# Kernel tuning notes

Hardware: AMD Instinct MI355X
Metric: run time of the kernel (lower is better)

The kernel has to match this reference:

```python
import jax, jax.numpy as jnp
import numpy as np

NS, NV = 48, 10
N_NODES, N_EDGES = 10000, 100000
N_EDGE_FEAT = 3 * NS  # 144
W_SS, W_VS, W_SV, W_VV = NS * NS, NV * NS, NS * NV, NV * NV
W_NUMEL = W_SS + W_VS + W_SV + W_VV  # 3364 = FullyConnectedTensorProduct.weight_numel
IN_DIM = NS + 3 * NV  # 78
EPS = 1e-5


def setup_inputs() -> dict:
    key = jax.random.key(0)
    ks = jax.random.split(key, 8)
    return {
        "node_attr": jax.random.normal(ks[0], (N_NODES, IN_DIM), jnp.float32),
        "edge_attr": jax.random.normal(ks[1], (N_EDGES, N_EDGE_FEAT), jnp.float32),
        "edge_sh": jax.random.normal(ks[2], (N_EDGES, 4), jnp.float32),
        "fc1_w": jax.random.normal(ks[3], (N_EDGE_FEAT, N_EDGE_FEAT), jnp.float32) / np.sqrt(N_EDGE_FEAT).astype(np.float32),
        "fc1_b": jnp.zeros((N_EDGE_FEAT,), jnp.float32),
        "fc2_w": jax.random.normal(ks[4], (N_EDGE_FEAT, W_NUMEL), jnp.float32) / np.sqrt(N_EDGE_FEAT).astype(np.float32),
        "fc2_b": jnp.zeros((W_NUMEL,), jnp.float32),
        "bn_weight": jnp.ones((NS + NV,), jnp.float32),
        "bn_bias": jnp.zeros((NS,), jnp.float32),
        "edge_index": jax.random.randint(ks[5], (2, N_EDGES), 0, N_NODES),
    }


def reference(node_attr, edge_attr, edge_sh, fc1_w, fc1_b, fc2_w, fc2_b, bn_weight, bn_bias, edge_index):
    edge_src, edge_dst = edge_index[0], edge_index[1]
    # --- gather node feats per edge, split into irreps ---
    x = node_attr[edge_dst]                      # [E, 78]
    xs = x[:, :NS]                               # [E, 48]  scalars (0e)
    xv = x[:, NS:].reshape(-1, NV, 3)            # [E, 10, 3] vectors (1o)
    s0 = edge_sh[:, 0]                           # [E]     sh 0e
    s1 = edge_sh[:, 1:4]                         # [E, 3]  sh 1o

    # --- per-edge TP weights from edge MLP ---
    w = jax.nn.relu(edge_attr @ fc1_w + fc1_b) @ fc2_w + fc2_b  # [E, 3364]
    w_ss = w[:, :W_SS].reshape(-1, NS, NS)
    w_vs = w[:, W_SS:W_SS + W_VS].reshape(-1, NV, NS)
    w_sv = w[:, W_SS + W_VS:W_SS + W_VS + W_SV].reshape(-1, NS, NV)
    w_vv = w[:, W_SS + W_VS + W_SV:].reshape(-1, NV, NV)

    # path normalization: 1/sqrt(mul_in * n_paths_into_output_irrep)
    a_ss = 1.0 / np.sqrt(NS * 2.0)
    a_vs = 1.0 / np.sqrt(NV * 2.0)
    a_sv = 1.0 / np.sqrt(NS * 2.0)
    a_vv = 1.0 / np.sqrt(NV * 2.0)

    # --- Clebsch-Gordan tensor product (fully connected, per-edge weights) ---
    # 0e (x) 0e -> 0e
    out_s = a_ss * jnp.einsum('ei,eio->eo', xs, w_ss) * s0[:, None]
    # 1o (x) 1o -> 0e  (CG = delta/sqrt(3))
    dot = jnp.einsum('eic,ec->ei', xv, s1) / np.sqrt(3.0)
    out_s = out_s + a_vs * jnp.einsum('ei,eio->eo', dot, w_vs)
    # 0e (x) 1o -> 1o
    out_v = a_sv * jnp.einsum('ei,eio->eo', xs, w_sv)[:, :, None] * s1[:, None, :]
    # 1o (x) 0e -> 1o
    out_v = out_v + a_vv * jnp.einsum('eic,eio->eoc', xv, w_vv) * s0[:, None, None]

    tp = jnp.concatenate([out_s, out_v.reshape(-1, 3 * NV)], axis=1)  # [E, 78]

    # --- scatter-mean to nodes ---
    sums = jax.ops.segment_sum(tp, edge_src, num_segments=N_NODES)
    cnt = jax.ops.segment_sum(jnp.ones((tp.shape[0],), tp.dtype), edge_src, num_segments=N_NODES)
    out = sums / jnp.maximum(cnt, 1.0)[:, None]

    # --- residual (in_dim == out_dim -> pad is a no-op) ---
    out = out + node_attr

    # --- equivariant batch norm (e3nn-style, batch statistics) ---
    os = out[:, :NS]
    ov = out[:, NS:].reshape(-1, NV, 3)
    mu = os.mean(0)
    var = os.var(0)
    os = (os - mu) / jnp.sqrt(var + EPS) * bn_weight[:NS] + bn_bias
    fn = (ov ** 2).sum(-1).mean(0) / 3.0  # component-normalized mean squared norm per channel
    ov = ov / jnp.sqrt(fn + EPS)[None, :, None] * bn_weight[NS:][None, :, None]
    return jnp.concatenate([os, ov.reshape(-1, 3 * NV)], axis=1)
```

## Files before the change

kernel.cpp:

```cpp
#include <hip/hip_runtime.h>
#include <hip/hip_bf16.h>

#define NS   48
#define NV   10
#define NEF  144
#define WN   3364
#define IND  78
#define NE   100000
#define NN   10000
#define EPS  1e-5f
#define HP   144
#define EB   128

#define A_SS 0.10206207261596575f
#define A_VS 0.22360679774997896f
#define A_SV 0.10206207261596575f
#define A_VV 0.22360679774997896f
#define RS3  0.5773502691896258f

typedef __attribute__((ext_vector_type(8)))  short  short8;
typedef __attribute__((ext_vector_type(16))) float  f32x16;
typedef __attribute__((ext_vector_type(4)))  int    int4v;
typedef __attribute__((ext_vector_type(4)))  float  float4v;
typedef __attribute__((ext_vector_type(2)))  float  float2v;

#define MFMA32(a,b,c) __builtin_amdgcn_mfma_f32_32x32x16_bf16((a),(b),(c),0,0,0)

#define TP_F    0
#define ST_F    7800000
#define CNT_F   7800160
#define OFFS_F  7810160
#define CUR_F   7820164
#define EL_F    7830164
#define WSBF_F  7930168

#define OFF_W1  0
#define OFF_B1  23040
#define OFF_B2  468480
#define OFF_B3  561664
#define N_PREP  608256

__device__ __forceinline__ short tobf(float v) {
    return __builtin_bit_cast(short, __float2bfloat16(v));
}
__device__ __forceinline__ float fromb(short s) {
    unsigned u = ((unsigned)(unsigned short)s) << 16;
    return __builtin_bit_cast(float, u);
}
__device__ __forceinline__ unsigned pkt2(float a, float b) {
    unsigned ua = __builtin_bit_cast(unsigned, a);
    unsigned ub = __builtin_bit_cast(unsigned, b);
    return (ua >> 16) | (ub & 0xFFFF0000u);
}
__device__ __forceinline__ float waveReduceSum(float v) {
    #pragma unroll
    for (int o = 32; o > 0; o >>= 1) v += __shfl_down(v, o, 64);
    return v;
}
__device__ __forceinline__ void gl_lds16(const short* g, short* l) {
    __builtin_amdgcn_global_load_lds(
        (const __attribute__((address_space(1))) unsigned int*)g,
        (__attribute__((address_space(3))) unsigned int*)l, 16, 0, 0);
}

__global__ void prep_weights(const float* __restrict__ fc1_w,
                             const float* __restrict__ fc2_w,
                             const float* __restrict__ b2,
                             short* __restrict__ wsbf)
{
    int idx = blockIdx.x * 256 + threadIdx.x;
    if (idx >= N_PREP) return;
    float v = 0.f;
    if (idx < OFF_B1) {
        int r = idx;
        int tile = r / 4608, rem = r % 4608;
        int ks = rem / 512, l = (rem % 512) / 8, j = rem % 8;
        int n = tile * 32 + (l & 31);
        int k = ks * 16 + ((l >> 5) << 3) + j;
        v = (n < 144) ? fc1_w[k * 144 + n] : 0.f;
    } else if (idx < OFF_B2) {
        int r = idx - OFF_B1;
        if (r < 442368) {
            int i = r / 9216, rem = r % 9216;
            int tile = rem / 4608; rem %= 4608;
            int ks = rem / 512, l = (rem % 512) / 8, j = rem % 8;
            int n = tile * 32 + (l & 31);
            int k = ks * 16 + ((l >> 5) << 3) + j;
            if (n < 48)      v = fc2_w[(size_t)k * WN + i * 48 + n];
            else if (n < 58) v = fc2_w[(size_t)k * WN + 2784 + i * 10 + (n - 48)];
        } else {
            int rb = r - 442368;
            int tile = rb / 1536, rem = rb % 1536;
            int ks = rem / 512, l = (rem % 512) / 8, j = rem % 8;
            int n = tile * 32 + (l & 31);
            int k = ks * 16 + ((l >> 5) << 3) + j;
            if (n < 48)      v = b2[k * 48 + n];
            else if (n < 58) v = b2[2784 + k * 10 + (n - 48)];
        }
    } else if (idx < OFF_B3) {
        int r = idx - OFF_B2;
        if (r < 92160) {
            int i = r / 9216, rem = r % 9216;
            int tile = rem / 4608; rem %= 4608;
            int ks = rem / 512, l = (rem % 512) / 8, j = rem % 8;
            int n = tile * 32 + (l & 31);
            int k = ks * 16 + ((l >> 5) << 3) + j;
            if (n < 48) v = fc2_w[(size_t)k * WN + 2304 + i * 48 + n];
        } else {
            int rb = r - 92160;
            int tile = rb / 512, rem = rb % 512;
            int l = rem / 8, j = rem % 8;
            int n = tile * 32 + (l & 31);
            int k = ((l >> 5) << 3) + j;
            if (k < 10 && n < 48) v = b2[2304 + k * 48 + n];
        }
    } else {
        int r = idx - OFF_B3;
        if (r < 46080) {
            int i = r / 4608, rem = r % 4608;
            int ks = rem / 512, l = (rem % 512) / 8, j = rem % 8;
            int n = l & 31;
            int k = ks * 16 + ((l >> 5) << 3) + j;
            if (n < 10) v = fc2_w[(size_t)k * WN + 3264 + i * 10 + n];
        } else {
            int rb = r - 46080;
            int l = rb / 8, j = rb % 8;
            int n = l & 31;
            int k = ((l >> 5) << 3) + j;
            if (k < 10 && n < 10) v = b2[3264 + k * 10 + n];
        }
    }
    wsbf[idx] = tobf(v);
}

__global__ void hist_kernel(const int* __restrict__ eidx, int* __restrict__ cntI)
{
    int e = blockIdx.x * 256 + threadIdx.x;
    if (e < NE) atomicAdd(&cntI[eidx[e]], 1);
}

__global__ __launch_bounds__(1024) void scan_kernel(const int* __restrict__ cntI,
                                                    int* __restrict__ offs,
                                                    int* __restrict__ cursor)
{
    __shared__ int part[1024];
    int t = threadIdx.x;
    int base = t * 10;
    int local[10];
    int s = 0;
    #pragma unroll
    for (int q = 0; q < 10; ++q) {
        int i = base + q;
        int v = (i < NN) ? cntI[i] : 0;
        local[q] = s; s += v;
    }
    part[t] = s;
    __syncthreads();
    for (int o = 1; o < 1024; o <<= 1) {
        int v = (t >= o) ? part[t - o] : 0;
        __syncthreads();
        part[t] += v;
        __syncthreads();
    }
    int prev = (t == 0) ? 0 : part[t - 1];
    #pragma unroll
    for (int q = 0; q < 10; ++q) {
        int i = base + q;
        if (i < NN) { int val = prev + local[q]; offs[i] = val; cursor[i] = val; }
    }
    if (t == 1023) offs[NN] = part[1023];
}

__global__ void scatter_kernel(const int* __restrict__ eidx,
                               int* __restrict__ cursor, int* __restrict__ elist)
{
    int e = blockIdx.x * 256 + threadIdx.x;
    if (e < NE) {
        int pos = atomicAdd(&cursor[eidx[e]], 1);
        elist[pos] = e;
    }
}

__global__ __launch_bounds__(256, 2) void fused_main(
    const float* __restrict__ node_attr, const float* __restrict__ edge_attr,
    const float* __restrict__ edge_sh,   const float* __restrict__ b1,
    const int*   __restrict__ eidx,      const short* __restrict__ wsbf,
    float* __restrict__ tp)
{
    __shared__ short ubuf[18432];
    __shared__ short xfT[96 * EB];
    __shared__ float pbuf[EB][10];
    __shared__ float s0s[EB];
    __shared__ float s1s[EB][3];

    const int t    = threadIdx.x;
    const int e0   = blockIdx.x * EB;
    const int lane = t & 63, wave = t >> 6;
    const int n32  = lane & 31, kh = lane >> 5;
    const int eL   = 32 * wave + n32;
    const int eLc  = min(e0 + eL, NE - 1);

    const short* W1L = wsbf + OFF_W1 + lane * 8;
    const short* B1L = wsbf + OFF_B1 + lane * 8;
    const short* B2L = wsbf + OFF_B2 + lane * 8;
    const short* B3L = wsbf + OFF_B3 + lane * 8;

    auto stageB = [&](const short* src, short* dst, int nfrag) {
        for (int f = wave; f < nfrag; f += 4)
            gl_lds16(src + f * 512 + lane * 8, dst + f * 512);
    };

    for (int idx = t; idx < 8 * EB; idx += 256) xfT[88 * EB + idx] = 0;

    if (t < EB) {
        int ee = e0 + t;
        if (ee < NE) {
            float4v sh = *reinterpret_cast<const float4v*>(edge_sh + (size_t)ee * 4);
            s0s[t] = sh.x; s1s[t][0] = sh.y; s1s[t][1] = sh.z; s1s[t][2] = sh.w;
        } else {
            s0s[t] = 0.f; s1s[t][0] = s1s[t][1] = s1s[t][2] = 0.f;
        }
    }

    {
        const int eg  = t & (EB - 1);
        const int jb  = t >> 7;
        const int egc = min(e0 + eg, NE - 1);
        const int dst = eidx[NE + egc];
        const float* na = node_attr + (size_t)dst * IND;
        for (int j = jb; j < IND; j += 2) {
            int slot = (j < NS) ? j : 58 + ((j - NS) % 3) * 10 + (j - NS) / 3;
            xfT[slot * EB + eg] = tobf(na[j]);
        }
    }

    short8 afc[9];
    {
        const float* ea = edge_attr + (size_t)eLc * NEF + kh * 8;
        #pragma unroll
        for (int ks = 0; ks < 9; ++ks) {
            float4v lo = *reinterpret_cast<const float4v*>(ea + ks * 16);
            float4v hi = *reinterpret_cast<const float4v*>(ea + ks * 16 + 4);
            int4v v = { (int)pkt2(lo.x, lo.y), (int)pkt2(lo.z, lo.w),
                        (int)pkt2(hi.x, hi.y), (int)pkt2(hi.z, hi.w) };
            afc[ks] = __builtin_bit_cast(short8, v);
        }
    }
    __syncthreads();

    #pragma unroll
    for (int it = 0; it < 5; ++it) {
        int e = t & (EB - 1);
        int i = (t >> 7) + 2 * it;
        float d = fromb(xfT[(58 + i) * EB + e]) * s1s[e][0]
                + fromb(xfT[(68 + i) * EB + e]) * s1s[e][1]
                + fromb(xfT[(78 + i) * EB + e]) * s1s[e][2];
        xfT[(48 + i) * EB + e] = tobf(d * RS3);
    }

    for (int pass = 0; pass < 3; ++pass) {
        int ntA = 2 * pass, ntB = 2 * pass + 1;
        bool hasB = (pass < 2);
        f32x16 accA = 0, accB = 0;
        #pragma unroll
        for (int ks = 0; ks < 9; ++ks) {
            short8 bA = *(const short8*)(W1L + (ntA * 9 + ks) * 512);
            accA = MFMA32(afc[ks], bA, accA);
            if (hasB) {
                short8 bB = *(const short8*)(W1L + (ntB * 9 + ks) * 512);
                accB = MFMA32(afc[ks], bB, accB);
            }
        }
        int colA = ntA * 32 + n32, colB = ntB * 32 + n32;
        float b1A = (colA < NEF) ? b1[colA] : 0.f;
        float b1B = (hasB && colB < NEF) ? b1[colB] : 0.f;
        #pragma unroll
        for (int r = 0; r < 16; ++r) {
            int row = (r & 3) + 8 * (r >> 2) + 4 * kh;
            int e = 32 * wave + row;
            if (colA < NEF) ubuf[e * HP + colA] = tobf(fmaxf(accA[r] + b1A, 0.f));
            if (hasB)       ubuf[e * HP + colB] = tobf(fmaxf(accB[r] + b1B, 0.f));
        }
    }

    float2v hreg[36];
    #pragma unroll
    for (int ks = 0; ks < 9; ++ks) {
        int4v hh = *(const int4v*)(ubuf + eL * HP + ks * 16 + kh * 8);
        #pragma unroll
        for (int q = 0; q < 4; ++q) {
            unsigned u = (unsigned)hh[q];
            float2v p;
            p.x = __builtin_bit_cast(float, u << 16);
            p.y = __builtin_bit_cast(float, u & 0xFFFF0000u);
            hreg[ks * 4 + q] = p;
        }
    }
    __syncthreads();

    short* stg0 = ubuf;
    short* stg1 = ubuf + 9216;

    stageB(wsbf + OFF_B1, stg0, 18);
    __syncthreads();

    auto genA = [&](float xv, int ks) -> short8 {
        float2v x2; x2.x = xv; x2.y = xv;
        int4v v;
        #pragma unroll
        for (int q = 0; q < 4; ++q) {
            float2v pr = hreg[ks * 4 + q] * x2;
            v[q] = (int)pkt2(pr.x, pr.y);
        }
        return __builtin_bit_cast(short8, v);
    };

    f32x16 acc1a = 0, acc1b = 0, acc2a = 0, acc2b = 0;
    {
        #pragma unroll 1
        for (int i = 0; i < 48; ++i) {
            short* cur = (i & 1) ? stg1 : stg0;
            short* nxt = (i & 1) ? stg0 : stg1;
            if (i < 47) stageB(wsbf + OFF_B1 + (i + 1) * 9216, nxt, 18);
            else        stageB(wsbf + OFF_B2, nxt, 18);
            float xv = fromb(xfT[i * EB + eL]);
            #pragma unroll
            for (int ks = 0; ks < 9; ++ks) {
                short8 a  = genA(xv, ks);
                short8 b0 = *(const short8*)(cur + ks * 512 + lane * 8);
                short8 b1f= *(const short8*)(cur + 4608 + ks * 512 + lane * 8);
                acc1a = MFMA32(a, b0, acc1a);
                acc1b = MFMA32(a, b1f, acc1b);
            }
            __syncthreads();
        }
        #pragma unroll
        for (int ks = 0; ks < 3; ++ks) {
            short8 a;
            #pragma unroll
            for (int j = 0; j < 8; ++j)
                a[j] = xfT[(ks * 16 + kh * 8 + j) * EB + eL];
            short8 b0 = *(const short8*)(B1L + 442368 + ks * 512);
            short8 b1f= *(const short8*)(B1L + 442368 + 1536 + ks * 512);
            acc1a = MFMA32(a, b0, acc1a);
            acc1b = MFMA32(a, b1f, acc1b);
        }
    }
    {
        #pragma unroll 1
        for (int i = 0; i < 10; ++i) {
            short* cur = (i & 1) ? stg1 : stg0;
            short* nxt = (i & 1) ? stg0 : stg1;
            if (i < 9) stageB(wsbf + OFF_B2 + (i + 1) * 9216, nxt, 18);
            else       stageB(wsbf + OFF_B3, nxt, 9);
            float xv = fromb(xfT[(48 + i) * EB + eL]);
            #pragma unroll
            for (int ks = 0; ks < 9; ++ks) {
                short8 a  = genA(xv, ks);
                short8 b0 = *(const short8*)(cur + ks * 512 + lane * 8);
                short8 b1f= *(const short8*)(cur + 4608 + ks * 512 + lane * 8);
                acc2a = MFMA32(a, b0, acc2a);
                acc2b = MFMA32(a, b1f, acc2b);
            }
            __syncthreads();
        }
        {
            short8 a;
            #pragma unroll
            for (int j = 0; j < 8; ++j)
                a[j] = xfT[(48 + kh * 8 + j) * EB + eL];
            short8 b0 = *(const short8*)(B2L + 92160);
            short8 b1f= *(const short8*)(B2L + 92160 + 512);
            acc2a = MFMA32(a, b0, acc2a);
            acc2b = MFMA32(a, b1f, acc2b);
        }
    }
    #pragma unroll
    for (int r = 0; r < 16; ++r) {
        int row = (r & 3) + 8 * (r >> 2) + 4 * kh;
        int e = 32 * wave + row;
        int ge = e0 + e;
        if (ge < NE) {
            float s0e = s0s[e];
            float* rowp = tp + (size_t)ge * IND;
            rowp[n32] = A_SS * s0e * acc1a[r] + A_VS * acc2a[r];
            int col = 32 + n32;
            if (col < 48) {
                rowp[col] = A_SS * s0e * acc1b[r] + A_VS * acc2b[r];
            } else if (col < 58) {
                pbuf[e][col - 48] = A_SV * acc1b[r];
            }
        }
    }
    {
        f32x16 acc30 = 0, acc31 = 0, acc32 = 0;
        #pragma unroll 1
        for (int i = 0; i < 10; ++i) {
            short* cur = (i & 1) ? stg1 : stg0;
            short* nxt = (i & 1) ? stg0 : stg1;
            if (i < 9) stageB(wsbf + OFF_B3 + (i + 1) * 4608, nxt, 9);
            float xv0 = fromb(xfT[(58 + i) * EB + eL]);
            float xv1 = fromb(xfT[(68 + i) * EB + eL]);
            float xv2 = fromb(xfT[(78 + i) * EB + eL]);
            #pragma unroll
            for (int ks = 0; ks < 9; ++ks) {
                short8 b0 = *(const short8*)(cur + ks * 512 + lane * 8);
                acc30 = MFMA32(genA(xv0, ks), b0, acc30);
                acc31 = MFMA32(genA(xv1, ks), b0, acc31);
                acc32 = MFMA32(genA(xv2, ks), b0, acc32);
            }
            __syncthreads();
        }
        {
            short8 bb = *(const short8*)(B3L + 46080);
            short8 a;
            #pragma unroll
            for (int j = 0; j < 8; ++j) a[j] = xfT[(58 + kh * 8 + j) * EB + eL];
            acc30 = MFMA32(a, bb, acc30);
            #pragma unroll
            for (int j = 0; j < 8; ++j) a[j] = xfT[(68 + kh * 8 + j) * EB + eL];
            acc31 = MFMA32(a, bb, acc31);
            #pragma unroll
            for (int j = 0; j < 8; ++j) a[j] = xfT[(78 + kh * 8 + j) * EB + eL];
            acc32 = MFMA32(a, bb, acc32);
        }
        if (n32 < 10) {
            #pragma unroll
            for (int r = 0; r < 16; ++r) {
                int row = (r & 3) + 8 * (r >> 2) + 4 * kh;
                int e = 32 * wave + row;
                int ge = e0 + e;
                if (ge < NE) {
                    float p  = pbuf[e][n32];
                    float qs = A_VV * s0s[e];
                    size_t base = (size_t)ge * IND + 48 + n32 * 3;
                    tp[base + 0] = p * s1s[e][0] + qs * acc30[r];
                    tp[base + 1] = p * s1s[e][1] + qs * acc31[r];
                    tp[base + 2] = p * s1s[e][2] + qs * acc32[r];
                }
            }
        }
    }
}

__global__ __launch_bounds__(256) void gather_kernel(const float* __restrict__ tp,
                                                     const int* __restrict__ offs,
                                                     const int* __restrict__ elist,
                                                     const float* __restrict__ node_attr,
                                                     float* __restrict__ out)
{
    int node = blockIdx.x * 4 + (threadIdx.x >> 6);
    int lane = threadIdx.x & 63;
    if (node >= NN) return;
    int beg = offs[node], end = offs[node + 1];
    float a0 = 0.f, a1 = 0.f;
    for (int p = beg; p < end; ++p) {
        int e = elist[p];
        const float* row = tp + (size_t)e * IND;
        a0 += row[lane];
        if (lane < 14) a1 += row[64 + lane];
    }
    float c = fmaxf((float)(end - beg), 1.0f);
    size_t base = (size_t)node * IND;
    out[base + lane] = a0 / c + node_attr[base + lane];
    if (lane < 14) out[base + 64 + lane] = a1 / c + node_attr[base + 64 + lane];
}

__global__ __launch_bounds__(256) void stats_kernel(const float* __restrict__ pre,
                                                    const float* __restrict__ bnw,
                                                    float* __restrict__ stats)
{
    int j = blockIdx.x;
    int t = threadIdx.x;
    float s1 = 0.f, s2 = 0.f;
    if (j < NS) {
        for (int n = t; n < NN; n += 256) {
            float v = pre[(size_t)n * IND + j];
            s1 += v; s2 += v * v;
        }
    } else {
        int vch = j - NS;
        for (int n = t; n < NN; n += 256) {
            float a = pre[(size_t)n * IND + NS + vch * 3 + 0];
            float b = pre[(size_t)n * IND + NS + vch * 3 + 1];
            float d = pre[(size_t)n * IND + NS + vch * 3 + 2];
            s2 += a * a + b * b + d * d;
        }
    }
    __shared__ float r1[4], r2[4];
    s1 = waveReduceSum(s1);
    s2 = waveReduceSum(s2);
    int w = t >> 6, lane = t & 63;
    if (lane == 0) { r1[w] = s1; r2[w] = s2; }
    __syncthreads();
    if (t == 0) {
        float S1 = r1[0] + r1[1] + r1[2] + r1[3];
        float S2 = r2[0] + r2[1] + r2[2] + r2[3];
        if (j < NS) {
            float mu  = S1 / (float)NN;
            float var = S2 / (float)NN - mu * mu;
            stats[j]      = mu;
            stats[64 + j] = bnw[j] * rsqrtf(var + EPS);
        } else {
            int vch = j - NS;
            float fn = S2 / (3.0f * (float)NN);
            stats[128 + vch] = bnw[j] * rsqrtf(fn + EPS);
        }
    }
}

__global__ void normalize_kernel(const float* __restrict__ stats,
                                 const float* __restrict__ bnb,
                                 float* __restrict__ out)
{
    int idx = blockIdx.x * 256 + threadIdx.x;
    if (idx >= NN * IND) return;
    int j = idx % IND;
    float x = out[idx];
    if (j < NS) out[idx] = (x - stats[j]) * stats[64 + j] + bnb[j];
    else        out[idx] = x * stats[128 + (j - NS) / 3];
}

extern "C" void kernel_launch(void* const* d_in, const int* in_sizes, int n_in,
                              void* d_out, int out_size, void* d_ws, size_t ws_size,
                              hipStream_t stream)
{
    (void)in_sizes; (void)n_in; (void)out_size; (void)ws_size;
    const float* node_attr = (const float*)d_in[0];
    const float* edge_attr = (const float*)d_in[1];
    const float* edge_sh   = (const float*)d_in[2];
    const float* fc1_w     = (const float*)d_in[3];
    const float* fc1_b     = (const float*)d_in[4];
    const float* fc2_w     = (const float*)d_in[5];
    const float* fc2_b     = (const float*)d_in[6];
    const float* bn_w      = (const float*)d_in[7];
    const float* bn_b      = (const float*)d_in[8];
    const int*   eidx      = (const int*)d_in[9];

    float* wsf   = (float*)d_ws;
    float* tp    = wsf + TP_F;
    float* stats = wsf + ST_F;
    int*   cntI  = (int*)(wsf + CNT_F);
    int*   offs  = (int*)(wsf + OFFS_F);
    int*   cur   = (int*)(wsf + CUR_F);
    int*   elist = (int*)(wsf + EL_F);
    short* wsbf  = (short*)(wsf + WSBF_F);
    float* out   = (float*)d_out;

    (void)hipMemsetAsync(cntI, 0, NN * sizeof(int), stream);
    prep_weights<<<(N_PREP + 255) / 256, 256, 0, stream>>>(fc1_w, fc2_w, fc2_b, wsbf);
    hist_kernel<<<(NE + 255) / 256, 256, 0, stream>>>(eidx, cntI);
    scan_kernel<<<1, 1024, 0, stream>>>(cntI, offs, cur);
    scatter_kernel<<<(NE + 255) / 256, 256, 0, stream>>>(eidx, cur, elist);
    fused_main<<<(NE + EB - 1) / EB, 256, 0, stream>>>(node_attr, edge_attr, edge_sh,
                                                       fc1_b, eidx, wsbf, tp);
    gather_kernel<<<(NN + 3) / 4, 256, 0, stream>>>(tp, offs, elist, node_attr, out);
    stats_kernel<<<NS + NV, 256, 0, stream>>>(out, bn_w, stats);
    normalize_kernel<<<(NN * IND + 255) / 256, 256, 0, stream>>>(stats, bn_b, out);
}
```

Before: 378.8 us.

## Single-buffer weight staging to cut LDS and raise occupancy to three blocks

```diff
diff --git a/kernel.cpp b/kernel.cpp
--- a/kernel.cpp
+++ b/kernel.cpp
@@ -9,7 +9,6 @@
 #define NE   100000
 #define NN   10000
 #define EPS  1e-5f
-#define HP   144
 #define EB   128
 
 #define A_SS 0.10206207261596575f
@@ -181,13 +180,13 @@
     }
 }
 
-__global__ __launch_bounds__(256, 2) void fused_main(
+__global__ __launch_bounds__(256, 3) void fused_main(
     const float* __restrict__ node_attr, const float* __restrict__ edge_attr,
     const float* __restrict__ edge_sh,   const float* __restrict__ b1,
     const int*   __restrict__ eidx,      const short* __restrict__ wsbf,
     float* __restrict__ tp)
 {
-    __shared__ short ubuf[18432];
+    __shared__ short stg[9216];
     __shared__ short xfT[96 * EB];
     __shared__ float pbuf[EB][10];
     __shared__ float s0s[EB];
@@ -205,9 +204,9 @@
     const short* B2L = wsbf + OFF_B2 + lane * 8;
     const short* B3L = wsbf + OFF_B3 + lane * 8;
 
-    auto stageB = [&](const short* src, short* dst, int nfrag) {
+    auto stageB = [&](const short* src, int nfrag) {
         for (int f = wave; f < nfrag; f += 4)
-            gl_lds16(src + f * 512 + lane * 8, dst + f * 512);
+            gl_lds16(src + f * 512 + lane * 8, stg + f * 512);
     };
 
     for (int idx = t; idx < 8 * EB; idx += 256) xfT[88 * EB + idx] = 0;
@@ -257,52 +256,55 @@
                 + fromb(xfT[(78 + i) * EB + e]) * s1s[e][2];
         xfT[(48 + i) * EB + e] = tobf(d * RS3);
     }
-
-    for (int pass = 0; pass < 3; ++pass) {
-        int ntA = 2 * pass, ntB = 2 * pass + 1;
-        bool hasB = (pass < 2);
-        f32x16 accA = 0, accB = 0;
-        #pragma unroll
-        for (int ks = 0; ks < 9; ++ks) {
-            short8 bA = *(const short8*)(W1L + (ntA * 9 + ks) * 512);
-            accA = MFMA32(afc[ks], bA, accA);
-            if (hasB) {
-                short8 bB = *(const short8*)(W1L + (ntB * 9 + ks) * 512);
-                accB = MFMA32(afc[ks], bB, accB);
-            }
-        }
-        int colA = ntA * 32 + n32, colB = ntB * 32 + n32;
-        float b1A = (colA < NEF) ? b1[colA] : 0.f;
-        float b1B = (hasB && colB < NEF) ? b1[colB] : 0.f;
-        #pragma unroll
-        for (int r = 0; r < 16; ++r) {
-            int row = (r & 3) + 8 * (r >> 2) + 4 * kh;
-            int e = 32 * wave + row;
-            if (colA < NEF) ubuf[e * HP + colA] = tobf(fmaxf(accA[r] + b1A, 0.f));
-            if (hasB)       ubuf[e * HP + colB] = tobf(fmaxf(accB[r] + b1B, 0.f));
-        }
-    }
+    __syncthreads();
 
     float2v hreg[36];
-    #pragma unroll
-    for (int ks = 0; ks < 9; ++ks) {
-        int4v hh = *(const int4v*)(ubuf + eL * HP + ks * 16 + kh * 8);
-        #pragma unroll
-        for (int q = 0; q < 4; ++q) {
-            unsigned u = (unsigned)hh[q];
-            float2v p;
-            p.x = __builtin_bit_cast(float, u << 16);
-            p.y = __builtin_bit_cast(float, u & 0xFFFF0000u);
-            hreg[ks * 4 + q] = p;
-        }
-    }
-    __syncthreads();
-
-    short* stg0 = ubuf;
-    short* stg1 = ubuf + 9216;
-
-    stageB(wsbf + OFF_B1, stg0, 18);
-    __syncthreads();
+    const int hrow = eL & 63;
+    #pragma unroll 1
+    for (int ph = 0; ph < 2; ++ph) {
+        if ((wave >> 1) == ph) {
+            for (int pass = 0; pass < 3; ++pass) {
+                int ntA = 2 * pass, ntB = 2 * pass + 1;
+                bool hasB = (pass < 2);
+                f32x16 accA = 0, accB = 0;
+                #pragma unroll
+                for (int ks = 0; ks < 9; ++ks) {
+                    short8 bA = *(const short8*)(W1L + (ntA * 9 + ks) * 512);
+                    accA = MFMA32(afc[ks], bA, accA);
+                    if (hasB) {
+                        short8 bB = *(const short8*)(W1L + (ntB * 9 + ks) * 512);
+                        accB = MFMA32(afc[ks], bB, accB);
+                    }
+                }
+                int colA = ntA * 32 + n32, colB = ntB * 32 + n32;
+                float b1A = (colA < NEF) ? b1[colA] : 0.f;
+                float b1B = (hasB && colB < NEF) ? b1[colB] : 0.f;
+                #pragma unroll
+                for (int r = 0; r < 16; ++r) {
+                    int row = (r & 3) + 8 * (r >> 2) + 4 * kh;
+                    int hr = 32 * (wave & 1) + row;
+                    if (colA < NEF) stg[hr * 144 + colA] = tobf(fmaxf(accA[r] + b1A, 0.f));
+                    if (hasB)       stg[hr * 144 + colB] = tobf(fmaxf(accB[r] + b1B, 0.f));
+                }
+            }
+        }
+        __syncthreads();
+        if ((wave >> 1) == ph) {
+            #pragma unroll
+            for (int ks = 0; ks < 9; ++ks) {
+                int4v hh = *(const int4v*)(stg + hrow * 144 + ks * 16 + kh * 8);
+                #pragma unroll
+                for (int q = 0; q < 4; ++q) {
+                    unsigned u = (unsigned)hh[q];
+                    float2v p;
+                    p.x = __builtin_bit_cast(float, u << 16);
+                    p.y = __builtin_bit_cast(float, u & 0xFFFF0000u);
+                    hreg[ks * 4 + q] = p;
+                }
+            }
+        }
+        __syncthreads();
+    }
 
     auto genA = [&](float xv, int ks) -> short8 {
         float2v x2; x2.x = xv; x2.y = xv;
@@ -316,64 +318,54 @@
     };
 
     f32x16 acc1a = 0, acc1b = 0, acc2a = 0, acc2b = 0;
-    {
-        #pragma unroll 1
-        for (int i = 0; i < 48; ++i) {
-            short* cur = (i & 1) ? stg1 : stg0;
-            short* nxt = (i & 1) ? stg0 : stg1;
-            if (i < 47) stageB(wsbf + OFF_B1 + (i + 1) * 9216, nxt, 18);
-            else        stageB(wsbf + OFF_B2, nxt, 18);
-            float xv = fromb(xfT[i * EB + eL]);
+    #pragma unroll 1
+    for (int i = 0; i < 58; ++i) {
+        const short* src = (i < 48) ? (wsbf + OFF_B1 + i * 9216)
+                                    : (wsbf + OFF_B2 + (i - 48) * 9216);
+        stageB(src, 18);
+        __syncthreads();
+        float xv = fromb(xfT[i * EB + eL]);
+        if (i < 48) {
             #pragma unroll
             for (int ks = 0; ks < 9; ++ks) {
                 short8 a  = genA(xv, ks);
-                short8 b0 = *(const short8*)(cur + ks * 512 + lane * 8);
-                short8 b1f= *(const short8*)(cur + 4608 + ks * 512 + lane * 8);
+                short8 b0 = *(const short8*)(stg + ks * 512 + lane * 8);
+                short8 b1f= *(const short8*)(stg + 4608 + ks * 512 + lane * 8);
                 acc1a = MFMA32(a, b0, acc1a);
                 acc1b = MFMA32(a, b1f, acc1b);
             }
-            __syncthreads();
-        }
-        #pragma unroll
-        for (int ks = 0; ks < 3; ++ks) {
-            short8 a;
-            #pragma unroll
-            for (int j = 0; j < 8; ++j)
-                a[j] = xfT[(ks * 16 + kh * 8 + j) * EB + eL];
-            short8 b0 = *(const short8*)(B1L + 442368 + ks * 512);
-            short8 b1f= *(const short8*)(B1L + 442368 + 1536 + ks * 512);
-            acc1a = MFMA32(a, b0, acc1a);
-            acc1b = MFMA32(a, b1f, acc1b);
-        }
-    }
-    {
-        #pragma unroll 1
-        for (int i = 0; i < 10; ++i) {
-            short* cur = (i & 1) ? stg1 : stg0;
-            short* nxt = (i & 1) ? stg0 : stg1;
-            if (i < 9) stageB(wsbf + OFF_B2 + (i + 1) * 9216, nxt, 18);
-            else       stageB(wsbf + OFF_B3, nxt, 9);
-            float xv = fromb(xfT[(48 + i) * EB + eL]);
+        } else {
             #pragma unroll
             for (int ks = 0; ks < 9; ++ks) {
                 short8 a  = genA(xv, ks);
-                short8 b0 = *(const short8*)(cur + ks * 512 + lane * 8);
-                short8 b1f= *(const short8*)(cur + 4608 + ks * 512 + lane * 8);
+                short8 b0 = *(const short8*)(stg + ks * 512 + lane * 8);
+                short8 b1f= *(const short8*)(stg + 4608 + ks * 512 + lane * 8);
                 acc2a = MFMA32(a, b0, acc2a);
                 acc2b = MFMA32(a, b1f, acc2b);
             }
-            __syncthreads();
-        }
-        {
-            short8 a;
-            #pragma unroll
-            for (int j = 0; j < 8; ++j)
-                a[j] = xfT[(48 + kh * 8 + j) * EB + eL];
-            short8 b0 = *(const short8*)(B2L + 92160);
-            short8 b1f= *(const short8*)(B2L + 92160 + 512);
-            acc2a = MFMA32(a, b0, acc2a);
-            acc2b = MFMA32(a, b1f, acc2b);
-        }
+        }
+        __syncthreads();
+    }
+    #pragma unroll
+    for (int ks = 0; ks < 3; ++ks) {
+        short8 a;
+        #pragma unroll
+        for (int j = 0; j < 8; ++j)
+            a[j] = xfT[(ks * 16 + kh * 8 + j) * EB + eL];
+        short8 b0 = *(const short8*)(B1L + 442368 + ks * 512);
+        short8 b1f= *(const short8*)(B1L + 442368 + 1536 + ks * 512);
+        acc1a = MFMA32(a, b0, acc1a);
+        acc1b = MFMA32(a, b1f, acc1b);
+    }
+    {
+        short8 a;
+        #pragma unroll
+        for (int j = 0; j < 8; ++j)
+            a[j] = xfT[(48 + kh * 8 + j) * EB + eL];
+        short8 b0 = *(const short8*)(B2L + 92160);
+        short8 b1f= *(const short8*)(B2L + 92160 + 512);
+        acc2a = MFMA32(a, b0, acc2a);
+        acc2b = MFMA32(a, b1f, acc2b);
     }
     #pragma unroll
     for (int r = 0; r < 16; ++r) {
@@ -396,15 +388,14 @@
         f32x16 acc30 = 0, acc31 = 0, acc32 = 0;
         #pragma unroll 1
         for (int i = 0; i < 10; ++i) {
-            short* cur = (i & 1) ? stg1 : stg0;
-            short* nxt = (i & 1) ? stg0 : stg1;
-            if (i < 9) stageB(wsbf + OFF_B3 + (i + 1) * 4608, nxt, 9);
+            stageB(wsbf + OFF_B3 + i * 4608, 9);
+            __syncthreads();
             float xv0 = fromb(xfT[(58 + i) * EB + eL]);
             float xv1 = fromb(xfT[(68 + i) * EB + eL]);
             float xv2 = fromb(xfT[(78 + i) * EB + eL]);
             #pragma unroll
             for (int ks = 0; ks < 9; ++ks) {
-                short8 b0 = *(const short8*)(cur + ks * 512 + lane * 8);
+                short8 b0 = *(const short8*)(stg + ks * 512 + lane * 8);
                 acc30 = MFMA32(genA(xv0, ks), b0, acc30);
                 acc31 = MFMA32(genA(xv1, ks), b0, acc31);
                 acc32 = MFMA32(genA(xv2, ks), b0, acc32);
```

After: 1.099 ms. +190.3%, slower.

## Split batch-norm stats into parallel slab accumulation plus finalize kernel

Applied to the files above, without the earlier changes.

```diff
diff --git a/kernel.cpp b/kernel.cpp
--- a/kernel.cpp
+++ b/kernel.cpp
@@ -29,10 +29,11 @@
 #define TP_F    0
 #define ST_F    7800000
 #define CNT_F   7800160
-#define OFFS_F  7810160
-#define CUR_F   7820164
-#define EL_F    7830164
-#define WSBF_F  7930168
+#define RAW_F   7810160
+#define OFFS_F  7810288
+#define CUR_F   7820292
+#define EL_F    7830292
+#define WSBF_F  7930292
 
 #define OFF_W1  0
 #define OFF_B1  23040
@@ -50,7 +51,7 @@
 __device__ __forceinline__ unsigned pkt2(float a, float b) {
     unsigned ua = __builtin_bit_cast(unsigned, a);
     unsigned ub = __builtin_bit_cast(unsigned, b);
-    return (ua >> 16) | (ub & 0xFFFF0000u);
+    return __builtin_amdgcn_perm(ub, ua, 0x07060302u);
 }
 __device__ __forceinline__ float waveReduceSum(float v) {
     #pragma unroll
@@ -466,46 +467,43 @@
     if (lane < 14) out[base + 64 + lane] = a1 / c + node_attr[base + 64 + lane];
 }
 
-__global__ __launch_bounds__(256) void stats_kernel(const float* __restrict__ pre,
-                                                    const float* __restrict__ bnw,
-                                                    float* __restrict__ stats)
-{
-    int j = blockIdx.x;
+#define SLAB 250
+__global__ __launch_bounds__(256) void stats_accum(const float* __restrict__ pre,
+                                                   float* __restrict__ raw)
+{
+    __shared__ float acc[112];
     int t = threadIdx.x;
-    float s1 = 0.f, s2 = 0.f;
-    if (j < NS) {
-        for (int n = t; n < NN; n += 256) {
-            float v = pre[(size_t)n * IND + j];
-            s1 += v; s2 += v * v;
-        }
-    } else {
-        int vch = j - NS;
-        for (int n = t; n < NN; n += 256) {
-            float a = pre[(size_t)n * IND + NS + vch * 3 + 0];
-            float b = pre[(size_t)n * IND + NS + vch * 3 + 1];
-            float d = pre[(size_t)n * IND + NS + vch * 3 + 2];
-            s2 += a * a + b * b + d * d;
-        }
-    }
-    __shared__ float r1[4], r2[4];
-    s1 = waveReduceSum(s1);
-    s2 = waveReduceSum(s2);
-    int w = t >> 6, lane = t & 63;
-    if (lane == 0) { r1[w] = s1; r2[w] = s2; }
+    if (t < 112) acc[t] = 0.f;
     __syncthreads();
-    if (t == 0) {
-        float S1 = r1[0] + r1[1] + r1[2] + r1[3];
-        float S2 = r2[0] + r2[1] + r2[2] + r2[3];
+    size_t base = (size_t)blockIdx.x * SLAB * IND;
+    for (int idx = t; idx < SLAB * IND; idx += 256) {
+        float v = pre[base + idx];
+        int j = idx % IND;
         if (j < NS) {
-            float mu  = S1 / (float)NN;
-            float var = S2 / (float)NN - mu * mu;
-            stats[j]      = mu;
-            stats[64 + j] = bnw[j] * rsqrtf(var + EPS);
+            atomicAdd(&acc[j], v);
+            atomicAdd(&acc[48 + j], v * v);
         } else {
-            int vch = j - NS;
-            float fn = S2 / (3.0f * (float)NN);
-            stats[128 + vch] = bnw[j] * rsqrtf(fn + EPS);
-        }
+            atomicAdd(&acc[96 + (j - NS) / 3], v * v);
+        }
+    }
+    __syncthreads();
+    if (t < 112) atomicAdd(&raw[t], acc[t]);
+}
+
+__global__ void stats_final(const float* __restrict__ raw,
+                            const float* __restrict__ bnw,
+                            float* __restrict__ stats)
+{
+    int t = threadIdx.x;
+    if (t < NS) {
+        float mu  = raw[t] / (float)NN;
+        float var = raw[48 + t] / (float)NN - mu * mu;
+        stats[t]      = mu;
+        stats[64 + t] = bnw[t] * rsqrtf(var + EPS);
+    }
+    if (t < NV) {
+        float fn = raw[96 + t] / (3.0f * (float)NN);
+        stats[128 + t] = bnw[NS + t] * rsqrtf(fn + EPS);
     }
 }
 
@@ -541,13 +539,14 @@
     float* tp    = wsf + TP_F;
     float* stats = wsf + ST_F;
     int*   cntI  = (int*)(wsf + CNT_F);
+    float* raw   = wsf + RAW_F;
     int*   offs  = (int*)(wsf + OFFS_F);
     int*   cur   = (int*)(wsf + CUR_F);
     int*   elist = (int*)(wsf + EL_F);
     short* wsbf  = (short*)(wsf + WSBF_F);
     float* out   = (float*)d_out;
 
-    (void)hipMemsetAsync(cntI, 0, NN * sizeof(int), stream);
+    (void)hipMemsetAsync(cntI, 0, (NN + 128) * sizeof(int), stream);
     prep_weights<<<(N_PREP + 255) / 256, 256, 0, stream>>>(fc1_w, fc2_w, fc2_b, wsbf);
     hist_kernel<<<(NE + 255) / 256, 256, 0, stream>>>(eidx, cntI);
     scan_kernel<<<1, 1024, 0, stream>>>(cntI, offs, cur);
@@ -555,6 +554,7 @@
     fused_main<<<(NE + EB - 1) / EB, 256, 0, stream>>>(node_attr, edge_attr, edge_sh,
                                                        fc1_b, eidx, wsbf, tp);
     gather_kernel<<<(NN + 3) / 4, 256, 0, stream>>>(tp, offs, elist, node_attr, out);
-    stats_kernel<<<NS + NV, 256, 0, stream>>>(out, bn_w, stats);
+    stats_accum<<<NN / SLAB, 256, 0, stream>>>(out, raw);
+    stats_final<<<1, 64, 0, stream>>>(raw, bn_w, stats);
     normalize_kernel<<<(NN * IND + 255) / 256, 256, 0, stream>>>(stats, bn_b, out);
 }
```

After: 389.2 us. 2.7% more time.
